# Optimization experiments

Hardware: AMD Instinct MI355X
Metric: run time of the kernel (lower is better)

Reference implementation:

```python
import jax, jax.numpy as jnp
import numpy as np

B, T, D = 4, 1024, 512
H, TD = 4, 5
DH = D // H          # per-head value dim
DFF = D // 2         # Clifford FFN half-width
DR = D               # reservoir size
M = 64               # 2**mem_depth leaves
OFFSETS = (-3, -2, -1, 0)  # causal sheaf window=3
EPS = 1e-5

def _ln(x, g, b):
    m = jnp.mean(x, axis=-1, keepdims=True)
    v = jnp.mean((x - m) ** 2, axis=-1, keepdims=True)
    return (x - m) / jnp.sqrt(v + EPS) * g + b

def setup_inputs() -> dict:
    keys = iter(jax.random.split(jax.random.key(0), 64))
    def rn(shape, s=0.02):
        return (jax.random.normal(next(keys), shape) * s).astype(jnp.float32)
    x = jax.random.normal(next(keys), (B, T, D), dtype=jnp.float32)
    # sparse reservoir recurrence matrix (sparsity=0.9)
    wres_mask = (jax.random.uniform(next(keys), (DR, DR)) > 0.9).astype(jnp.float32)
    res_Wres = jax.random.normal(next(keys), (DR, DR)) * wres_mask * 0.05
    eye = jnp.eye(D, dtype=jnp.float32)
    sheaf_Rw = jnp.stack([eye + rn((D, D), 0.01) for _ in OFFSETS])  # [4,D,D]
    return dict(
        x=x,
        ln1_g=jnp.ones((D,)), ln1_b=jnp.zeros((D,)),
        ln2_g=jnp.ones((D,)), ln2_b=jnp.zeros((D,)),
        ln3_g=jnp.ones((D,)), ln3_b=jnp.zeros((D,)),
        ln4_g=jnp.ones((D,)), ln4_b=jnp.zeros((D,)),
        attn_Wp=rn((H * TD, D)), attn_bp=jnp.zeros((H * TD,)),
        attn_Wv=rn((D, D)), attn_Wo=rn((D, D)),
        ffn_Wr=rn((DFF, D)), ffn_br=jnp.zeros((DFF,)),
        ffn_Wi=rn((DFF, D)), ffn_bi=jnp.zeros((DFF,)),
        ffn_Wg=rn((D, D)), ffn_bg=jnp.zeros((D,)),
        ffn_Wout=rn((D, D)), ffn_bout=jnp.zeros((D,)),
        res_Win=rn((DR, D)), res_Wres=res_Wres,
        res_logrho=jnp.float32(0.0), res_leak=jnp.float32(0.3),
        res_readout=rn((D, DR)),
        res_v0=jax.random.normal(next(keys), (DR,), dtype=jnp.float32),
        mem_keys=rn((M, D)), mem_vals=rn((M, D)),
        mem_Wq=rn((D, D)), mem_Wout=rn((D, D)), mem_bout=jnp.zeros((D,)),
        sheaf_Rw=sheaf_Rw, sheaf_Rb=jnp.zeros((len(OFFSETS), D)),
        sheaf_alpha=jnp.float32(0.15),
    )

def reference(x, ln1_g, ln1_b, ln2_g, ln2_b, ln3_g, ln3_b, ln4_g, ln4_b,
              attn_Wp, attn_bp, attn_Wv, attn_Wo,
              ffn_Wr, ffn_br, ffn_Wi, ffn_bi, ffn_Wg, ffn_bg, ffn_Wout, ffn_bout,
              res_Win, res_Wres, res_logrho, res_leak, res_readout, res_v0,
              mem_keys, mem_vals, mem_Wq, mem_Wout, mem_bout,
              sheaf_Rw, sheaf_Rb, sheaf_alpha):
    Bx, Tx, d = x.shape

    def attn_fn(h):  # PAdicAttention, causal
        paths = jax.nn.sigmoid(h @ attn_Wp.T + attn_bp)
        paths = paths.reshape(Bx, Tx, H, TD).transpose(0, 2, 1, 3)   # [B,H,T,TD]
        pq = paths[:, :, :, None, :]
        pk = paths[:, :, None, :, :]
        agree = pq * pk + (1.0 - pq) * (1.0 - pk)                    # [B,H,T,T,TD]
        sim = jnp.sum(jnp.cumprod(agree, axis=-1), axis=-1) / TD     # [B,H,T,T]
        mask = jnp.triu(jnp.ones((Tx, Tx), bool), 1)
        sim = jnp.where(mask[None, None], -jnp.inf, sim)
        a = jax.nn.softmax(sim, axis=-1)
        V = (h @ attn_Wv.T).reshape(Bx, Tx, H, DH).transpose(0, 2, 1, 3)
        ctx = jnp.einsum('bhqk,bhkd->bhqd', a, V)
        return ctx.transpose(0, 2, 1, 3).reshape(Bx, Tx, d) @ attn_Wo.T

    def res_fn(h):  # EchoStateReservoir
        rho_t = jax.nn.sigmoid(res_logrho) * 1.5
        Wd = jax.lax.stop_gradient(res_Wres)
        def pi(v, _):
            v = Wd @ v
            n = jnp.linalg.norm(v)
            return jnp.where(n > 0, v / n, v), None
        v, _ = jax.lax.scan(pi, res_v0, None, length=3)
        rho_c = jax.lax.stop_gradient(jnp.linalg.norm(Wd @ v))
        Ws = res_Wres * (rho_t / jnp.maximum(rho_c, 1e-6))
        lk = jax.nn.sigmoid(res_leak)
        u = h @ res_Win.T                                            # [B,T,dr]
        def step(hs, ut):
            hs = (1.0 - lk) * hs + lk * jnp.tanh(hs @ Ws.T + ut)
            return hs, hs
        _, Hs = jax.lax.scan(step, jnp.zeros((Bx, DR), x.dtype), u.transpose(1, 0, 2))
        return Hs.transpose(1, 0, 2) @ res_readout.T

    def mem_fn(h):  # PAdicMemory
        q = h @ mem_Wq.T
        w = jax.nn.softmax(q @ mem_keys.T / jnp.sqrt(jnp.float32(d)), axis=-1)
        return (w @ mem_vals) @ mem_Wout.T + mem_bout

    def ffn_fn(h):  # CliffordFFN
        r = h @ ffn_Wr.T + ffn_br
        i = h @ ffn_Wi.T + ffn_bi
        prod = jnp.concatenate([r * r - i * i, 2.0 * r * i], axis=-1)
        gate = jax.nn.sigmoid(h @ ffn_Wg.T + ffn_bg)
        return (prod * gate) @ ffn_Wout.T + ffn_bout

    def sheaf_fn(h):  # SheafDiffusion, causal offsets
        lap = jnp.zeros_like(h)
        for idx, delta in enumerate(OFFSETS):
            Rx = h @ sheaf_Rw[idx].T + sheaf_Rb[idx]
            if delta == 0:
                x_nb = h
            else:
                ad = -delta
                x_nb = jnp.concatenate(
                    [jnp.zeros((Bx, ad, d), h.dtype), h[:, :Tx - ad, :]], axis=1)
            lap = lap + (Rx - x_nb) @ sheaf_Rw[idx]   # note: @ W, not W.T (as in source)
        return h - jnp.abs(sheaf_alpha) * lap

    x = x + attn_fn(_ln(x, ln1_g, ln1_b))
    x = x + res_fn(_ln(x, ln2_g, ln2_b))
    x = x + mem_fn(_ln(x, ln3_g, ln3_b))
    x = x + ffn_fn(_ln(x, ln4_g, ln4_b))
    return sheaf_fn(x)
```

## Files before the change

### kernel.cpp

```cpp
#include <hip/hip_runtime.h>
#include <hip/hip_bf16.h>
#include <stdint.h>

typedef unsigned short u16;
typedef unsigned int u32;
typedef unsigned long long u64;
typedef __bf16 bf16x8 __attribute__((ext_vector_type(8)));
typedef float f32x4 __attribute__((ext_vector_type(4)));
typedef int i32x4 __attribute__((ext_vector_type(4)));

__device__ __forceinline__ u16 f2bf(float f){
  unsigned u = __float_as_uint(f);
  u += 0x7fffu + ((u>>16)&1u);
  return (u16)(u>>16);
}
__device__ __forceinline__ float sigm(float x){ return 1.f/(1.f+__expf(-x)); }
__device__ __forceinline__ float tanh_fast(float x){ float e = __expf(2.f*x); return 1.f - 2.f/(e+1.f); }

__device__ __forceinline__ void gl_lds16(const void* g, void* l){
  __builtin_amdgcn_global_load_lds((const __attribute__((address_space(1))) void*)g,
                                   (__attribute__((address_space(3))) void*)l, 16, 0, 0);
}

__global__ __launch_bounds__(128) void prep_weights(
  const float* Wp, const float* Wv, const float* Wo, const float* Win, const float* rd,
  const float* Wq, const float* keys, const float* vals, const float* mWo,
  const float* Wr, const float* Wi, const float* Wg, const float* fWo, const float* Rw,
  const float* bp, const float* fbr, const float* fbi, const float* fbg,
  u16* WpB, u16* WvB, u16* WoB, u16* WinB, u16* rdB,
  u16* WqB, u16* keysB, u16* valsB, u16* mWoB,
  u16* WrB, u16* WiB, u16* WgB, u16* fWoB, u16* RwB,
  float* bpp, float* bpc, float* ss)
{
  int blk = blockIdx.x, t = threadIdx.x;
  if(blk==6912){ if(t<128) bpp[t] = (t<20)? bp[t] : 0.f; return; }
  if(blk==6913){
    for(int j=t; j<1024; j+=128)
      bpc[j] = (j<256)? fbr[j] : (j<512)? fbi[j-256] : fbg[j-512];
    return;
  }
  if(blk==6914){ if(t==0) ss[0]=1.f; else if(t<5) ss[t]=0.f; return; }
  const float* src = nullptr; u16* dst = nullptr; int r;
  if(blk<128){ r=blk; dst=WpB+(size_t)r*512; if(r<20) src=Wp+(size_t)r*512; }
  else if(blk<640){ r=blk-128; dst=WvB+(size_t)r*512; src=Wv+(size_t)r*512; }
  else if(blk<1152){ r=blk-640; dst=WoB+(size_t)r*512; src=Wo+(size_t)r*512; }
  else if(blk<1664){ r=blk-1152; dst=WinB+(size_t)r*512; src=Win+(size_t)r*512; }
  else if(blk<2176){ r=blk-1664; dst=rdB+(size_t)r*512; src=rd+(size_t)r*512; }
  else if(blk<2688){ r=blk-2176; dst=WqB+(size_t)r*512; src=Wq+(size_t)r*512; }
  else if(blk<2752){ r=blk-2688; dst=keysB+(size_t)r*512; src=keys+(size_t)r*512; }
  else if(blk<2816){ r=blk-2752; dst=valsB+(size_t)r*512; src=vals+(size_t)r*512; }
  else if(blk<3328){ r=blk-2816; dst=mWoB+(size_t)r*512; src=mWo+(size_t)r*512; }
  else if(blk<3584){ r=blk-3328; dst=WrB+(size_t)r*512; src=Wr+(size_t)r*512; }
  else if(blk<3840){ r=blk-3584; dst=WiB+(size_t)r*512; src=Wi+(size_t)r*512; }
  else if(blk<4352){ r=blk-3840; dst=WgB+(size_t)r*512; src=Wg+(size_t)r*512; }
  else if(blk<4864){ r=blk-4352; dst=fWoB+(size_t)r*512; src=fWo+(size_t)r*512; }
  else { r=blk-4864; dst=RwB+(size_t)r*512; src=Rw+(size_t)r*512; }
  if(src){
    float4 a = *(const float4*)&src[t*4];
    ushort4 o; o.x=f2bf(a.x); o.y=f2bf(a.y); o.z=f2bf(a.z); o.w=f2bf(a.w);
    *(ushort4*)&dst[t*4] = o;
  } else {
    ushort4 z; z.x=0; z.y=0; z.z=0; z.w=0;
    *(ushort4*)&dst[t*4] = z;
  }
}

__global__ __launch_bounds__(256) void transpose_rw(const float* __restrict__ Rw, u16* __restrict__ RwT){
  __shared__ float tl[32][33];
  int z = blockIdx.z, it = blockIdx.x, jt = blockIdx.y;
  const float* src = Rw + (size_t)z*262144;
  u16* dst = RwT + (size_t)z*262144;
  int r = threadIdx.x>>3, c4 = (threadIdx.x&7)*4;
  float4 v = *(const float4*)&src[(size_t)(jt*32+r)*512 + it*32 + c4];
  tl[r][c4+0]=v.x; tl[r][c4+1]=v.y; tl[r][c4+2]=v.z; tl[r][c4+3]=v.w;
  __syncthreads();
  ushort4 o;
  o.x = f2bf(tl[c4+0][r]); o.y = f2bf(tl[c4+1][r]);
  o.z = f2bf(tl[c4+2][r]); o.w = f2bf(tl[c4+3][r]);
  *(ushort4*)&dst[(size_t)(it*32+r)*512 + jt*32 + c4] = o;
}

__global__ __launch_bounds__(64) void ln_kernel(const float* __restrict__ x, const float* __restrict__ g,
      const float* __restrict__ b, u16* __restrict__ out)
{
  int row = blockIdx.x, lane = threadIdx.x;
  const float* xr = x + (size_t)row*512;
  float4 v0 = *(const float4*)&xr[lane*4];
  float4 v1 = *(const float4*)&xr[256+lane*4];
  float s = v0.x+v0.y+v0.z+v0.w + v1.x+v1.y+v1.z+v1.w;
  float q = v0.x*v0.x+v0.y*v0.y+v0.z*v0.z+v0.w*v0.w + v1.x*v1.x+v1.y*v1.y+v1.z*v1.z+v1.w*v1.w;
  #pragma unroll
  for(int m=1;m<64;m<<=1){ s += __shfl_xor(s,m); q += __shfl_xor(q,m); }
  float mean = s*(1.f/512.f);
  float var  = q*(1.f/512.f) - mean*mean;
  float rstd = rsqrtf(var + 1e-5f);
  float4 g0 = *(const float4*)&g[lane*4], g1 = *(const float4*)&g[256+lane*4];
  float4 b0 = *(const float4*)&b[lane*4], b1 = *(const float4*)&b[256+lane*4];
  ushort4 o0, o1;
  o0.x = f2bf((v0.x-mean)*rstd*g0.x + b0.x); o0.y = f2bf((v0.y-mean)*rstd*g0.y + b0.y);
  o0.z = f2bf((v0.z-mean)*rstd*g0.z + b0.z); o0.w = f2bf((v0.w-mean)*rstd*g0.w + b0.w);
  o1.x = f2bf((v1.x-mean)*rstd*g1.x + b1.x); o1.y = f2bf((v1.y-mean)*rstd*g1.y + b1.y);
  o1.z = f2bf((v1.z-mean)*rstd*g1.z + b1.z); o1.w = f2bf((v1.w-mean)*rstd*g1.w + b1.w);
  *(ushort4*)&out[(size_t)row*512 + lane*4] = o0;
  *(ushort4*)&out[(size_t)row*512 + 256 + lane*4] = o1;
}

template<int EPI>
__global__ __launch_bounds__(256,2) void gemm_nt(
  const u16* __restrict__ A, const u16* __restrict__ Bw, int K, int ldc,
  float* __restrict__ outf, u16* __restrict__ outb,
  const float* __restrict__ bias, const float* __restrict__ resid,
  const float* __restrict__ aux, float* __restrict__ outf2,
  const float* __restrict__ scal, int shift_ad)
{
  __shared__ u16 Al[128*64];
  __shared__ u16 Bl[64*64];
  const int t = threadIdx.x;
  const int bm = blockIdx.x, bn = blockIdx.y;
  const int wid = t>>6, lane = t&63;
  const int wr = wid>>1, wc = wid&1;
  const int fr = lane&15, fq = lane>>4;
  f32x4 acc[4][2] = {};
  const int nK = K>>6;
  const u16* Ab = A + (size_t)(bm*128)*K;
  const u16* Bb = Bw + (size_t)(bn*64)*K;
  const int srow8 = t>>3;
  const int scol = (t&7)*8;
  char* AlB = (char*)Al; char* BlB = (char*)Bl;
  const int lbase = wid*1024;
  for(int bk=0; bk<nK; ++bk){
    #pragma unroll
    for(int c=0;c<4;++c)
      gl_lds16(&Ab[(size_t)(c*32+srow8)*K + bk*64 + scol], AlB + c*4096 + lbase);
    #pragma unroll
    for(int c=0;c<2;++c)
      gl_lds16(&Bb[(size_t)(c*32+srow8)*K + bk*64 + scol], BlB + c*4096 + lbase);
    __syncthreads();
    #pragma unroll
    for(int kk=0;kk<2;++kk){
      bf16x8 af[4], bf[2];
      #pragma unroll
      for(int m=0;m<4;++m) af[m] = *(const bf16x8*)&Al[(wr*64+m*16+fr)*64 + kk*32 + fq*8];
      #pragma unroll
      for(int n=0;n<2;++n) bf[n] = *(const bf16x8*)&Bl[(wc*32+n*16+fr)*64 + kk*32 + fq*8];
      #pragma unroll
      for(int m=0;m<4;++m)
        #pragma unroll
        for(int n=0;n<2;++n)
          acc[m][n] = __builtin_amdgcn_mfma_f32_16x16x32_bf16(af[m], bf[n], acc[m][n], 0,0,0);
    }
    __syncthreads();
  }
  float alpha = 0.f;
  if(EPI==8) alpha = fabsf(scal[0]);
  #pragma unroll
  for(int m=0;m<4;++m){
    int gr0 = bm*128 + wr*64 + m*16 + fq*4;
    #pragma unroll
    for(int n=0;n<2;++n){
      int gc = bn*64 + wc*32 + n*16 + fr;
      float bv = 0.f;
      if(EPI==2||EPI==3||EPI==5||EPI==6||EPI==7||EPI==9) bv = bias[gc];
      if(EPI==10 && gc<128) bv = bias[gc];
      #pragma unroll
      for(int i=0;i<4;++i){
        int r = gr0 + i;
        float v = acc[m][n][i] + bv;
        if(EPI==3) v = sigm(v);
        if(EPI==1||EPI==5||EPI==6) v += resid[(size_t)r*ldc + gc];
        if(EPI==7){
          int ts = r & 1023;
          float xnb = (ts >= shift_ad) ? aux[(size_t)(r-shift_ad)*ldc + gc] : 0.f;
          v -= xnb;
        }
        if(EPI==8){
          outf[(size_t)r*ldc + gc] -= alpha*v;
        } else if(EPI==9){
          if(gc<512) outf[(size_t)r*512 + gc] = v;
          else       outf2[(size_t)r*512 + gc-512] = sigm(v);
        } else if(EPI==10){
          if(gc<128) outf[(size_t)r*128 + gc] = sigm(v);
          else       outf2[(size_t)r*512 + gc-128] = v;
        } else {
          if(EPI==0||EPI==1||EPI==2||EPI==3||EPI==5||EPI==6) outf[(size_t)r*ldc + gc] = v;
          if(EPI==6) outf2[(size_t)r*ldc + gc] = v;
          if(EPI==4||EPI==6||EPI==7) outb[(size_t)r*ldc + gc] = f2bf(v);
        }
      }
    }
  }
}

__global__ __launch_bounds__(128) void attn_kernel(
  const float* __restrict__ paths, const float* __restrict__ Vbuf, u16* __restrict__ ctxb)
{
  const int t = threadIdx.x;
  const int qt = blockIdx.x, bh = blockIdx.y;
  const int b = bh>>2, h = bh&3;
  const int rb = b<<10;
  const int ql = t>>2, sub = t&3;
  const int q = qt*32 + ql;
  const int wid = t>>6, lane = t&63;
  const int fr = lane&15, fq = lane>>4;
  __shared__ u16 Vl[128][72];
  __shared__ u16 Pl[32][72];
  __shared__ float pkl[64][6];
  __shared__ float scl[32];
  __shared__ float lsm[32];
  float al[5], bl[5];
  #pragma unroll
  for(int l=0;l<5;++l){
    float p = paths[(size_t)(rb+q)*128 + h*5 + l];
    al[l] = 2.f*p - 1.f; bl[l] = 1.f - p;
  }
  float m_run = -1e30f, l_run = 0.f;
  f32x4 acc[2][4] = {};
  const int nkt = (qt>>1) + 1;
  for(int kt=0; kt<nkt; ++kt){
    int k0 = kt*64;
    for(int i=t; i<320; i+=128){
      int k = i/5, l = i%5;
      pkl[k][l] = paths[(size_t)(rb+k0+k)*128 + h*5 + l];
    }
    {
      int dg = (t&31)*4, kbase = t>>5;
      #pragma unroll
      for(int i=0;i<16;++i){
        int k = kbase + i*4;
        float4 v4 = *(const float4*)&Vbuf[(size_t)(rb+k0+k)*512 + h*128 + dg];
        Vl[dg+0][k] = f2bf(v4.x); Vl[dg+1][k] = f2bf(v4.y);
        Vl[dg+2][k] = f2bf(v4.z); Vl[dg+3][k] = f2bf(v4.w);
      }
    }
    __syncthreads();
    float pj[16]; float tm = -1e30f;
    #pragma unroll
    for(int j=0;j<16;++j){
      int kidx = sub*16 + j;
      int k = k0 + kidx;
      float s;
      if(k <= q){
        float c = al[0]*pkl[kidx][0] + bl[0];
        float sa = c;
        #pragma unroll
        for(int l=1;l<5;++l){ c *= al[l]*pkl[kidx][l] + bl[l]; sa += c; }
        s = sa*0.2f;
      } else s = -1e30f;
      pj[j] = s; tm = fmaxf(tm, s);
    }
    tm = fmaxf(tm, __shfl_xor(tm,1,4));
    tm = fmaxf(tm, __shfl_xor(tm,2,4));
    float m_new = fmaxf(m_run, tm);
    float corr = __expf(m_run - m_new);
    float ls = 0.f;
    #pragma unroll
    for(int j=0;j<16;++j){
      float p = (pj[j] > -1e29f) ? __expf(pj[j]-m_new) : 0.f;
      ls += p;
      Pl[ql][sub*16+j] = f2bf(p);
    }
    l_run = l_run*corr + ls;
    m_run = m_new;
    if(sub==0) scl[ql] = corr;
    __syncthreads();
    #pragma unroll
    for(int m=0;m<2;++m){
      float c0 = scl[m*16+fq*4+0], c1 = scl[m*16+fq*4+1];
      float c2 = scl[m*16+fq*4+2], c3 = scl[m*16+fq*4+3];
      #pragma unroll
      for(int n=0;n<4;++n){ acc[m][n][0]*=c0; acc[m][n][1]*=c1; acc[m][n][2]*=c2; acc[m][n][3]*=c3; }
    }
    #pragma unroll
    for(int kk=0;kk<2;++kk){
      bf16x8 af[2], bf[4];
      #pragma unroll
      for(int m=0;m<2;++m) af[m] = *(const bf16x8*)&Pl[m*16+fr][kk*32+fq*8];
      #pragma unroll
      for(int n=0;n<4;++n) bf[n] = *(const bf16x8*)&Vl[wid*64+n*16+fr][kk*32+fq*8];
      #pragma unroll
      for(int m=0;m<2;++m)
        #pragma unroll
        for(int n=0;n<4;++n)
          acc[m][n] = __builtin_amdgcn_mfma_f32_16x16x32_bf16(af[m], bf[n], acc[m][n], 0,0,0);
    }
    __syncthreads();
  }
  {
    float lt = l_run + __shfl_xor(l_run,1,4);
    lt += __shfl_xor(lt,2,4);
    if(sub==0) lsm[ql] = lt;
  }
  __syncthreads();
  #pragma unroll
  for(int m=0;m<2;++m){
    float inv[4];
    #pragma unroll
    for(int i=0;i<4;++i) inv[i] = 1.f/lsm[m*16+fq*4+i];
    #pragma unroll
    for(int n=0;n<4;++n){
      int row = rb + qt*32 + m*16 + fq*4;
      int col = h*128 + wid*64 + n*16 + fr;
      #pragma unroll
      for(int i=0;i<4;++i)
        ctxb[(size_t)(row+i)*512 + col] = f2bf(acc[m][n][i]*inv[i]);
    }
  }
}

__global__ __launch_bounds__(256) void pmv(const float* __restrict__ W, const float* __restrict__ vin,
                    const float* __restrict__ ssin, float* __restrict__ vout, float* __restrict__ ssout)
{
  __shared__ float vs[512];
  int t = threadIdx.x;
  int j = blockIdx.x*16 + (t>>4), ks = t&15;
  float s = ssin[0];
  float inv = (s>0.f)? rsqrtf(s) : 1.f;
  vs[t] = vin[t]*inv; vs[t+256] = vin[t+256]*inv;
  __syncthreads();
  float p = 0.f;
  const float* wr = &W[(size_t)j*512 + ks*32];
  #pragma unroll
  for(int kk=0;kk<32;++kk) p += wr[kk]*vs[ks*32+kk];
  p += __shfl_xor(p,1,16); p += __shfl_xor(p,2,16); p += __shfl_xor(p,4,16); p += __shfl_xor(p,8,16);
  if(ks==0){ vout[j] = p; atomicAdd(ssout, p*p); }
}

__global__ __launch_bounds__(128) void scale_ws(const float* __restrict__ Wres, const float* __restrict__ ss4,
                         const float* __restrict__ logrho, signed char* __restrict__ WsQ,
                         float* __restrict__ wscale)
{
  __shared__ float wmax[2];
  int j = blockIdx.x, t = threadIdx.x;
  float rho_t = 1.5f * sigm(logrho[0]);
  float rho_c = sqrtf(ss4[0]);
  float sc = rho_t / fmaxf(rho_c, 1e-6f);
  float4 w = *(const float4*)&Wres[(size_t)j*512 + t*4];
  w.x*=sc; w.y*=sc; w.z*=sc; w.w*=sc;
  float m = fmaxf(fmaxf(fabsf(w.x),fabsf(w.y)), fmaxf(fabsf(w.z),fabsf(w.w)));
  #pragma unroll
  for(int d=1; d<64; d<<=1) m = fmaxf(m, __shfl_xor(m, d));
  if((t&63)==0) wmax[t>>6] = m;
  __syncthreads();
  float rm = fmaxf(wmax[0], wmax[1]);
  float qs = (rm > 0.f) ? rm*(1.f/127.f) : 1.f;
  float inv = 1.f/qs;
  int q0 = __float2int_rn(w.x*inv), q1 = __float2int_rn(w.y*inv);
  int q2 = __float2int_rn(w.z*inv), q3 = __float2int_rn(w.w*inv);
  q0 = min(127,max(-127,q0)); q1 = min(127,max(-127,q1));
  q2 = min(127,max(-127,q2)); q3 = min(127,max(-127,q3));
  u32 pk = (u32)(q0&0xff) | ((u32)(q1&0xff)<<8) | ((u32)(q2&0xff)<<16) | ((u32)(q3&0xff)<<24);
  *(u32*)&WsQ[(size_t)j*512 + t*4] = pk;
  if(t==0) wscale[j] = qs*(1.f/127.f);
}

__global__ __launch_bounds__(512) void scan_kernel(
  const signed char* __restrict__ WsQ, const float* __restrict__ wscale,
  const float* __restrict__ u, const float* __restrict__ leak_p,
  u16* __restrict__ HsB)
{
  const int t = threadIdx.x;
  const int w = t>>6, lane = t&63, fr = lane&15, fq = lane>>4;
  const int colb = w*64;
  const float lk = sigm(leak_p[0]);
  const float omlk = 1.f - lk;
  __shared__ signed char Sl[2][16*512];
  for(int i=t; i<4096; i+=512) ((u32*)Sl)[i] = 0u;
  float mysc[4];
  i32x4 bw[4][8];
  #pragma unroll
  for(int cg=0; cg<4; ++cg){
    int col = colb + cg*16 + fr;
    mysc[cg] = wscale[col];
    #pragma unroll
    for(int ks=0; ks<8; ++ks)
      bw[cg][ks] = *(const i32x4*)&WsQ[(size_t)col*512 + ks*64 + fq*16];
  }
  #pragma unroll
  for(int cg=0; cg<4; ++cg)
    #pragma unroll
    for(int ks=0; ks<8; ++ks)
      asm volatile("" : "+v"(bw[cg][ks]));
  float hp[4];
  #pragma unroll
  for(int cg=0;cg<4;++cg) hp[cg]=0.f;
  float uvc[4];
  #pragma unroll
  for(int cg=0;cg<4;++cg)
    uvc[cg] = u[(size_t)(fq*1024)*512 + colb + cg*16 + fr];
  const int rdswz = ((fr&3)<<4) ^ (((fr>>2)&3)<<6);
  const int wrswz = fq<<6;
  __syncthreads();
  for(int ts=0; ts<1024; ++ts){
    const int tn = (ts+1 < 1024) ? (ts+1) : 1023;
    float uvn[4];
    #pragma unroll
    for(int cg=0;cg<4;++cg)
      uvn[cg] = u[(size_t)(fq*1024 + tn)*512 + colb + cg*16 + fr];
    const signed char* Sb = Sl[ts&1];
    i32x4 af[8];
    #pragma unroll
    for(int ks=0; ks<8; ++ks)
      af[ks] = *(const i32x4*)&Sb[fr*512 + ((ks*64 + fq*16) ^ rdswz)];
    i32x4 accA[4], accB[4];
    #pragma unroll
    for(int cg=0;cg<4;++cg){ i32x4 z = {0,0,0,0}; accA[cg] = z; accB[cg] = z; }
    #pragma unroll
    for(int ks=0;ks<4;++ks)
      #pragma unroll
      for(int cg=0;cg<4;++cg){
        accA[cg] = __builtin_amdgcn_mfma_i32_16x16x64_i8(af[ks],   bw[cg][ks],   accA[cg], 0,0,0);
        accB[cg] = __builtin_amdgcn_mfma_i32_16x16x64_i8(af[ks+4], bw[cg][ks+4], accB[cg], 0,0,0);
      }
    signed char* So = Sl[(ts+1)&1];
    #pragma unroll
    for(int cg=0;cg<4;++cg){
      float pre = (float)(accA[cg][0] + accB[cg][0])*mysc[cg] + uvc[cg];
      float h = omlk*hp[cg] + lk*tanh_fast(pre);
      hp[cg] = h;
      int qi = __float2int_rn(h*127.f);
      qi = min(127, max(-127, qi));
      So[(4*fq)*512 + ((colb + cg*16 + fr) ^ wrswz)] = (signed char)qi;
      HsB[(size_t)(fq*1024+ts)*512 + colb + cg*16 + fr] = f2bf(h);
      uvc[cg] = uvn[cg];
    }
    asm volatile("s_waitcnt lgkmcnt(0)" ::: "memory");
    __builtin_amdgcn_s_barrier();
    asm volatile("" ::: "memory");
  }
}

__global__ __launch_bounds__(256) void mem_kernel(
  const u16* __restrict__ qb, const u16* __restrict__ keysB, const u16* __restrict__ valsB,
  u16* __restrict__ ctx2b)
{
  const int t = threadIdx.x, rt = blockIdx.x;
  const int wid = t>>6, lane = t&63, fr = lane&15, fq = lane>>4;
  __shared__ float S[64][65];
  __shared__ u16 Pl[64][72];
  __shared__ u16 VT[256][72];
  {
    f32x4 accs[4] = {};
    for(int ks=0; ks<16; ++ks){
      bf16x8 bfrag = *(const bf16x8*)&keysB[(size_t)(wid*16+fr)*512 + ks*32 + fq*8];
      #pragma unroll
      for(int mt=0;mt<4;++mt){
        bf16x8 afrag = *(const bf16x8*)&qb[(size_t)(rt*64+mt*16+fr)*512 + ks*32 + fq*8];
        accs[mt] = __builtin_amdgcn_mfma_f32_16x16x32_bf16(afrag, bfrag, accs[mt], 0,0,0);
      }
    }
    #pragma unroll
    for(int mt=0;mt<4;++mt)
      #pragma unroll
      for(int i=0;i<4;++i)
        S[mt*16+fq*4+i][wid*16+fr] = accs[mt][i];
  }
  __syncthreads();
  if(t<64){
    float m = -1e30f;
    for(int j=0;j<64;++j) m = fmaxf(m, S[t][j]);
    const float scale = 0.04419417382f;
    float sum = 0.f;
    for(int j=0;j<64;++j){ float p = __expf((S[t][j]-m)*scale); sum += p; S[t][j] = p; }
    float inv = 1.f/sum;
    for(int j=0;j<64;++j) Pl[t][j] = f2bf(S[t][j]*inv);
  }
  __syncthreads();
  for(int pass=0; pass<2; ++pass){
    {
      int k = t&63, cb = t>>6;
      #pragma unroll
      for(int i=0;i<8;++i){
        int d0 = (cb + i*4)*8;
        uint4 v = *(const uint4*)&valsB[(size_t)k*512 + pass*256 + d0];
        VT[d0+0][k]=(u16)(v.x); VT[d0+1][k]=(u16)(v.x>>16);
        VT[d0+2][k]=(u16)(v.y); VT[d0+3][k]=(u16)(v.y>>16);
        VT[d0+4][k]=(u16)(v.z); VT[d0+5][k]=(u16)(v.z>>16);
        VT[d0+6][k]=(u16)(v.w); VT[d0+7][k]=(u16)(v.w>>16);
      }
    }
    __syncthreads();
    f32x4 accp[4][4] = {};
    #pragma unroll
    for(int kk=0;kk<2;++kk){
      bf16x8 af[4], bf[4];
      #pragma unroll
      for(int mt=0;mt<4;++mt) af[mt] = *(const bf16x8*)&Pl[mt*16+fr][kk*32+fq*8];
      #pragma unroll
      for(int nt=0;nt<4;++nt) bf[nt] = *(const bf16x8*)&VT[wid*64+nt*16+fr][kk*32+fq*8];
      #pragma unroll
      for(int mt=0;mt<4;++mt)
        #pragma unroll
        for(int nt=0;nt<4;++nt)
          accp[mt][nt] = __builtin_amdgcn_mfma_f32_16x16x32_bf16(af[mt], bf[nt], accp[mt][nt], 0,0,0);
    }
    #pragma unroll
    for(int mt=0;mt<4;++mt)
      #pragma unroll
      for(int nt=0;nt<4;++nt){
        int row = rt*64 + mt*16 + fq*4;
        int col = pass*256 + wid*64 + nt*16 + fr;
        #pragma unroll
        for(int i=0;i<4;++i)
          ctx2b[(size_t)(row+i)*512 + col] = f2bf(accp[mt][nt][i]);
      }
    __syncthreads();
  }
}

__global__ __launch_bounds__(256) void prodgate(const float* __restrict__ ri, const float* __restrict__ g,
                         u16* __restrict__ pgb)
{
  int gi = blockIdx.x*256 + threadIdx.x;
  int row = gi>>7, c4 = (gi&127)*4;
  const float* base = ri + (size_t)row*512;
  float4 gv = *(const float4*)&g[(size_t)row*512 + c4];
  float4 o;
  if(c4 < 256){
    float4 r = *(const float4*)&base[c4];
    float4 ii = *(const float4*)&base[256+c4];
    o.x = (r.x*r.x - ii.x*ii.x)*gv.x; o.y = (r.y*r.y - ii.y*ii.y)*gv.y;
    o.z = (r.z*r.z - ii.z*ii.z)*gv.z; o.w = (r.w*r.w - ii.w*ii.w)*gv.w;
  } else {
    float4 r = *(const float4*)&base[c4-256];
    float4 ii = *(const float4*)&base[c4];
    o.x = 2.f*r.x*ii.x*gv.x; o.y = 2.f*r.y*ii.y*gv.y;
    o.z = 2.f*r.z*ii.z*gv.z; o.w = 2.f*r.w*ii.w*gv.w;
  }
  ushort4 us; us.x=f2bf(o.x); us.y=f2bf(o.y); us.z=f2bf(o.z); us.w=f2bf(o.w);
  *(ushort4*)&pgb[(size_t)row*512 + c4] = us;
}

static void launch_gemm(int epi, dim3 grid, const u16* A, const u16* B, int ldc,
  float* outf, u16* outb, const float* bias, const float* resid, const float* aux,
  float* outf2, const float* scal, int ad, hipStream_t s)
{
  switch(epi){
    case 0: gemm_nt<0><<<grid,256,0,s>>>(A,B,512,ldc,outf,outb,bias,resid,aux,outf2,scal,ad); break;
    case 1: gemm_nt<1><<<grid,256,0,s>>>(A,B,512,ldc,outf,outb,bias,resid,aux,outf2,scal,ad); break;
    case 2: gemm_nt<2><<<grid,256,0,s>>>(A,B,512,ldc,outf,outb,bias,resid,aux,outf2,scal,ad); break;
    case 3: gemm_nt<3><<<grid,256,0,s>>>(A,B,512,ldc,outf,outb,bias,resid,aux,outf2,scal,ad); break;
    case 4: gemm_nt<4><<<grid,256,0,s>>>(A,B,512,ldc,outf,outb,bias,resid,aux,outf2,scal,ad); break;
    case 5: gemm_nt<5><<<grid,256,0,s>>>(A,B,512,ldc,outf,outb,bias,resid,aux,outf2,scal,ad); break;
    case 6: gemm_nt<6><<<grid,256,0,s>>>(A,B,512,ldc,outf,outb,bias,resid,aux,outf2,scal,ad); break;
    case 7: gemm_nt<7><<<grid,256,0,s>>>(A,B,512,ldc,outf,outb,bias,resid,aux,outf2,scal,ad); break;
    case 8: gemm_nt<8><<<grid,256,0,s>>>(A,B,512,ldc,outf,outb,bias,resid,aux,outf2,scal,ad); break;
    case 9: gemm_nt<9><<<grid,256,0,s>>>(A,B,512,ldc,outf,outb,bias,resid,aux,outf2,scal,ad); break;
    case 10: gemm_nt<10><<<grid,256,0,s>>>(A,B,512,ldc,outf,outb,bias,resid,aux,outf2,scal,ad); break;
  }
}

extern "C" void kernel_launch(void* const* d_in, const int* in_sizes, int n_in,
                              void* d_out, int out_size, void* d_ws, size_t ws_size,
                              hipStream_t stream)
{
  const float* x      = (const float*)d_in[0];
  const float* ln1g   = (const float*)d_in[1];  const float* ln1b = (const float*)d_in[2];
  const float* ln2g   = (const float*)d_in[3];  const float* ln2b = (const float*)d_in[4];
  const float* ln3g   = (const float*)d_in[5];  const float* ln3b = (const float*)d_in[6];
  const float* ln4g   = (const float*)d_in[7];  const float* ln4b = (const float*)d_in[8];
  const float* aWp    = (const float*)d_in[9];  const float* abp  = (const float*)d_in[10];
  const float* aWv    = (const float*)d_in[11]; const float* aWo  = (const float*)d_in[12];
  const float* fWr    = (const float*)d_in[13]; const float* fbr  = (const float*)d_in[14];
  const float* fWi    = (const float*)d_in[15]; const float* fbi  = (const float*)d_in[16];
  const float* fWg    = (const float*)d_in[17]; const float* fbg  = (const float*)d_in[18];
  const float* fWo    = (const float*)d_in[19]; const float* fbo  = (const float*)d_in[20];
  const float* rWin   = (const float*)d_in[21]; const float* rWres= (const float*)d_in[22];
  const float* rlogr  = (const float*)d_in[23]; const float* rleak= (const float*)d_in[24];
  const float* rread  = (const float*)d_in[25]; const float* rv0  = (const float*)d_in[26];
  const float* mkeys  = (const float*)d_in[27]; const float* mvals= (const float*)d_in[28];
  const float* mWq    = (const float*)d_in[29]; const float* mWo  = (const float*)d_in[30];
  const float* mbo    = (const float*)d_in[31];
  const float* sRw    = (const float*)d_in[32]; const float* sRb  = (const float*)d_in[33];
  const float* salpha = (const float*)d_in[34];
  (void)in_sizes; (void)n_in; (void)out_size;

  char* ws = (char*)d_ws;
  float* XCUR  = (float*)(ws + 0);
  u16*   HB    = (u16*)  (ws + 8388608);
  float* VU    = (float*)(ws + 12582912);
  u16*   X4B   = (u16*)  (ws + 12582912);
  float* PATHS = (float*)(ws + 20971520);
  u16*   CTXB  = (u16*)  (ws + 23068672);
  u16*   HSB   = (u16*)  (ws + 27262976);
  char* WB = ws + 31457280;
  u16* WpB   = (u16*)(WB + 0);
  u16* WvB   = (u16*)(WB + 131072);
  u16* WoB   = (u16*)(WB + 655360);
  u16* WinB  = (u16*)(WB + 1179648);
  u16* rdB   = (u16*)(WB + 1703936);
  u16* WqB   = (u16*)(WB + 2228224);
  u16* keysB = (u16*)(WB + 2752512);
  u16* valsB = (u16*)(WB + 2818048);
  u16* mWoB  = (u16*)(WB + 2883584);
  u16* WrB   = (u16*)(WB + 3407872);
  u16* WiB   = (u16*)(WB + 3670016);
  u16* WgB   = (u16*)(WB + 3932160);
  u16* fWoB  = (u16*)(WB + 4456448);
  u16* RwB   = (u16*)(WB + 4980736);
  u16* RwTB  = (u16*)(WB + 7077888);
  signed char* WsQ = (signed char*)(WB + 9175040);
  float* wscale = (float*)(WB + 9437184);
  float* bpp = (float*)(WB + 9699328);
  float* bpc = (float*)(WB + 9699840);
  float* ssv = (float*)(WB + 9733632);
  float* vr  = (float*)(WB + 9733696);
  float* GATE = (float*)d_out;

  if(ws_size < (size_t)41200000) return;

  prep_weights<<<6915,128,0,stream>>>(aWp,aWv,aWo,rWin,rread,mWq,mkeys,mvals,mWo,fWr,fWi,fWg,fWo,sRw,
      abp, fbr, fbi, fbg,
      WpB,WvB,WoB,WinB,rdB,WqB,keysB,valsB,mWoB,WrB,WiB,WgB,fWoB,RwB,bpp,bpc,ssv);
  transpose_rw<<<dim3(16,16,4),256,0,stream>>>(sRw, RwTB);

  dim3 g512(32,8), g640(32,10), g1024(32,16);

  ln_kernel<<<4096,64,0,stream>>>(x, ln1g, ln1b, HB);
  launch_gemm(10, g640, HB, WpB, 0, PATHS, nullptr, bpp, nullptr, nullptr, VU, nullptr, 0, stream);
  attn_kernel<<<dim3(32,16),128,0,stream>>>(PATHS, VU, CTXB);
  launch_gemm(1, g512, CTXB, WoB, 512, XCUR, nullptr, nullptr, x, nullptr, nullptr, nullptr, 0, stream);

  ln_kernel<<<4096,64,0,stream>>>(XCUR, ln2g, ln2b, HB);
  launch_gemm(0, g512, HB, WinB, 512, VU, nullptr, nullptr, nullptr, nullptr, nullptr, nullptr, 0, stream);
  pmv<<<32,256,0,stream>>>(rWres, rv0,   &ssv[0], &vr[0],    &ssv[1]);
  pmv<<<32,256,0,stream>>>(rWres, &vr[0],   &ssv[1], &vr[512],  &ssv[2]);
  pmv<<<32,256,0,stream>>>(rWres, &vr[512], &ssv[2], &vr[1024], &ssv[3]);
  pmv<<<32,256,0,stream>>>(rWres, &vr[1024],&ssv[3], &vr[1536], &ssv[4]);
  scale_ws<<<512,128,0,stream>>>(rWres, &ssv[4], rlogr, WsQ, wscale);
  scan_kernel<<<1,512,0,stream>>>(WsQ, wscale, VU, rleak, HSB);
  launch_gemm(1, g512, HSB, rdB, 512, XCUR, nullptr, nullptr, XCUR, nullptr, nullptr, nullptr, 0, stream);

  ln_kernel<<<4096,64,0,stream>>>(XCUR, ln3g, ln3b, HB);
  launch_gemm(4, g512, HB, WqB, 512, nullptr, CTXB, nullptr, nullptr, nullptr, nullptr, nullptr, 0, stream);
  mem_kernel<<<64,256,0,stream>>>(CTXB, keysB, valsB, HSB);
  launch_gemm(5, g512, HSB, mWoB, 512, XCUR, nullptr, mbo, XCUR, nullptr, nullptr, nullptr, 0, stream);

  ln_kernel<<<4096,64,0,stream>>>(XCUR, ln4g, ln4b, HB);
  launch_gemm(9, g1024, HB, WrB, 0, VU, nullptr, bpc, nullptr, nullptr, GATE, nullptr, 0, stream);
  prodgate<<<2048,256,0,stream>>>(VU, GATE, CTXB);
  launch_gemm(6, g512, CTXB, fWoB, 512, XCUR, X4B, fbo, XCUR, nullptr, (float*)d_out, nullptr, 0, stream);

  const int ads[4] = {3,2,1,0};
  for(int idx=0; idx<4; ++idx){
    launch_gemm(7, g512, X4B, RwB + (size_t)idx*262144, 512,
                nullptr, CTXB, sRb + idx*512, nullptr, XCUR, nullptr, nullptr, ads[idx], stream);
    launch_gemm(8, g512, CTXB, RwTB + (size_t)idx*262144, 512,
                (float*)d_out, nullptr, nullptr, nullptr, nullptr, nullptr, salpha, 0, stream);
  }
}
```

Baseline: 1.352 ms.

## Batch sheaf diffusion into two wide GEMMs and vectorize reservoir scan I/O

The four per-offset pairs of sheaf GEMMs become one N=2048 GEMM that writes the shifted differences in bf16, followed by one K=2048 GEMM against a concatenated transposed Rw. This cuts the launch count and removes repeated read-modify-write passes over the fp32 output. The reservoir input projection and readout weights are column-permuted so the scan kernel can use float4 loads, packed int8 LDS stores and packed bf16 stores. The trade-off is that the neighbour term now comes from bf16 X4B instead of fp32 XCUR, which adds precision loss, and the change touches buffer aliasing.

```diff
diff --git a/kernel.cpp b/kernel.cpp
--- a/kernel.cpp
+++ b/kernel.cpp
@@ -14,6 +14,7 @@
   u += 0x7fffu + ((u>>16)&1u);
   return (u16)(u>>16);
 }
+__device__ __forceinline__ float bf2f(u16 h){ return __uint_as_float((u32)h<<16); }
 __device__ __forceinline__ float sigm(float x){ return 1.f/(1.f+__expf(-x)); }
 __device__ __forceinline__ float tanh_fast(float x){ float e = __expf(2.f*x); return 1.f - 2.f/(e+1.f); }
 
@@ -21,6 +22,7 @@
   __builtin_amdgcn_global_load_lds((const __attribute__((address_space(1))) void*)g,
                                    (__attribute__((address_space(3))) void*)l, 16, 0, 0);
 }
+
 
 __global__ __launch_bounds__(128) void prep_weights(
   const float* Wp, const float* Wv, const float* Wo, const float* Win, const float* rd,
@@ -41,11 +43,12 @@
   }
   if(blk==6914){ if(t==0) ss[0]=1.f; else if(t<5) ss[t]=0.f; return; }
   const float* src = nullptr; u16* dst = nullptr; int r;
+  bool perm = false;
   if(blk<128){ r=blk; dst=WpB+(size_t)r*512; if(r<20) src=Wp+(size_t)r*512; }
   else if(blk<640){ r=blk-128; dst=WvB+(size_t)r*512; src=Wv+(size_t)r*512; }
   else if(blk<1152){ r=blk-640; dst=WoB+(size_t)r*512; src=Wo+(size_t)r*512; }
   else if(blk<1664){ r=blk-1152; dst=WinB+(size_t)r*512; src=Win+(size_t)r*512; }
-  else if(blk<2176){ r=blk-1664; dst=rdB+(size_t)r*512; src=rd+(size_t)r*512; }
+  else if(blk<2176){ r=blk-1664; dst=rdB+(size_t)r*512; src=rd+(size_t)r*512; perm=true; }
   else if(blk<2688){ r=blk-2176; dst=WqB+(size_t)r*512; src=Wq+(size_t)r*512; }
   else if(blk<2752){ r=blk-2688; dst=keysB+(size_t)r*512; src=keys+(size_t)r*512; }
   else if(blk<2816){ r=blk-2752; dst=valsB+(size_t)r*512; src=vals+(size_t)r*512; }
@@ -58,7 +61,13 @@
   if(src){
     float4 a = *(const float4*)&src[t*4];
     ushort4 o; o.x=f2bf(a.x); o.y=f2bf(a.y); o.z=f2bf(a.z); o.w=f2bf(a.w);
-    *(ushort4*)&dst[t*4] = o;
+    if(perm){
+      int k0 = t*4;
+      int base = (k0 & ~63) | ((k0&15)<<2) | ((k0>>4)&3);
+      dst[base] = o.x; dst[base+4] = o.y; dst[base+8] = o.z; dst[base+12] = o.w;
+    } else {
+      *(ushort4*)&dst[t*4] = o;
+    }
   } else {
     ushort4 z; z.x=0; z.y=0; z.z=0; z.w=0;
     *(ushort4*)&dst[t*4] = z;
@@ -69,7 +78,6 @@
   __shared__ float tl[32][33];
   int z = blockIdx.z, it = blockIdx.x, jt = blockIdx.y;
   const float* src = Rw + (size_t)z*262144;
-  u16* dst = RwT + (size_t)z*262144;
   int r = threadIdx.x>>3, c4 = (threadIdx.x&7)*4;
   float4 v = *(const float4*)&src[(size_t)(jt*32+r)*512 + it*32 + c4];
   tl[r][c4+0]=v.x; tl[r][c4+1]=v.y; tl[r][c4+2]=v.z; tl[r][c4+3]=v.w;
@@ -77,7 +85,7 @@
   ushort4 o;
   o.x = f2bf(tl[c4+0][r]); o.y = f2bf(tl[c4+1][r]);
   o.z = f2bf(tl[c4+2][r]); o.w = f2bf(tl[c4+3][r]);
-  *(ushort4*)&dst[(size_t)(it*32+r)*512 + jt*32 + c4] = o;
+  *(ushort4*)&RwT[(size_t)(it*32+r)*2048 + z*512 + jt*32 + c4] = o;
 }
 
 __global__ __launch_bounds__(64) void ln_kernel(const float* __restrict__ x, const float* __restrict__ g,
@@ -160,7 +168,7 @@
     for(int n=0;n<2;++n){
       int gc = bn*64 + wc*32 + n*16 + fr;
       float bv = 0.f;
-      if(EPI==2||EPI==3||EPI==5||EPI==6||EPI==7||EPI==9) bv = bias[gc];
+      if(EPI==2||EPI==3||EPI==5||EPI==6||EPI==9||EPI==12) bv = bias[gc];
       if(EPI==10 && gc<128) bv = bias[gc];
       #pragma unroll
       for(int i=0;i<4;++i){
@@ -168,11 +176,6 @@
         float v = acc[m][n][i] + bv;
         if(EPI==3) v = sigm(v);
         if(EPI==1||EPI==5||EPI==6) v += resid[(size_t)r*ldc + gc];
-        if(EPI==7){
-          int ts = r & 1023;
-          float xnb = (ts >= shift_ad) ? aux[(size_t)(r-shift_ad)*ldc + gc] : 0.f;
-          v -= xnb;
-        }
         if(EPI==8){
           outf[(size_t)r*ldc + gc] -= alpha*v;
         } else if(EPI==9){
@@ -181,10 +184,20 @@
         } else if(EPI==10){
           if(gc<128) outf[(size_t)r*128 + gc] = sigm(v);
           else       outf2[(size_t)r*512 + gc-128] = v;
+        } else if(EPI==11){
+          int pc = (gc & ~63) | ((gc&15)<<2) | ((gc>>4)&3);
+          outf[(size_t)r*512 + pc] = v;
+        } else if(EPI==12){
+          int idx = gc>>9;
+          int ad = 3 - idx;
+          int ts = r & 1023;
+          float xnb = 0.f;
+          if(ts >= ad) xnb = bf2f(((const u16*)aux)[(size_t)(r-ad)*512 + (gc&511)]);
+          outb[(size_t)r*2048 + gc] = f2bf(v - xnb);
         } else {
-          if(EPI==0||EPI==1||EPI==2||EPI==3||EPI==5||EPI==6) outf[(size_t)r*ldc + gc] = v;
+          if(EPI==0||EPI==1||EPI==2||EPI==3||EPI==5) outf[(size_t)r*ldc + gc] = v;
           if(EPI==6) outf2[(size_t)r*ldc + gc] = v;
-          if(EPI==4||EPI==6||EPI==7) outb[(size_t)r*ldc + gc] = f2bf(v);
+          if(EPI==4||EPI==6) outb[(size_t)r*ldc + gc] = f2bf(v);
         }
       }
     }
@@ -331,12 +344,14 @@
 {
   __shared__ float wmax[2];
   int j = blockIdx.x, t = threadIdx.x;
+  int fr = t&15, blk = t>>4;
   float rho_t = 1.5f * sigm(logrho[0]);
   float rho_c = sqrtf(ss4[0]);
   float sc = rho_t / fmaxf(rho_c, 1e-6f);
-  float4 w = *(const float4*)&Wres[(size_t)j*512 + t*4];
-  w.x*=sc; w.y*=sc; w.z*=sc; w.w*=sc;
-  float m = fmaxf(fmaxf(fabsf(w.x),fabsf(w.y)), fmaxf(fabsf(w.z),fabsf(w.w)));
+  float w[4];
+  #pragma unroll
+  for(int cg=0;cg<4;++cg) w[cg] = Wres[(size_t)j*512 + blk*64 + cg*16 + fr]*sc;
+  float m = fmaxf(fmaxf(fabsf(w[0]),fabsf(w[1])), fmaxf(fabsf(w[2]),fabsf(w[3])));
   #pragma unroll
   for(int d=1; d<64; d<<=1) m = fmaxf(m, __shfl_xor(m, d));
   if((t&63)==0) wmax[t>>6] = m;
@@ -344,12 +359,12 @@
   float rm = fmaxf(wmax[0], wmax[1]);
   float qs = (rm > 0.f) ? rm*(1.f/127.f) : 1.f;
   float inv = 1.f/qs;
-  int q0 = __float2int_rn(w.x*inv), q1 = __float2int_rn(w.y*inv);
-  int q2 = __float2int_rn(w.z*inv), q3 = __float2int_rn(w.w*inv);
+  int q0 = __float2int_rn(w[0]*inv), q1 = __float2int_rn(w[1]*inv);
+  int q2 = __float2int_rn(w[2]*inv), q3 = __float2int_rn(w[3]*inv);
   q0 = min(127,max(-127,q0)); q1 = min(127,max(-127,q1));
   q2 = min(127,max(-127,q2)); q3 = min(127,max(-127,q3));
   u32 pk = (u32)(q0&0xff) | ((u32)(q1&0xff)<<8) | ((u32)(q2&0xff)<<16) | ((u32)(q3&0xff)<<24);
-  *(u32*)&WsQ[(size_t)j*512 + t*4] = pk;
+  *(u32*)&WsQ[(size_t)j*512 + blk*64 + fr*4] = pk;
   if(t==0) wscale[j] = qs*(1.f/127.f);
 }
 
@@ -383,19 +398,14 @@
   float hp[4];
   #pragma unroll
   for(int cg=0;cg<4;++cg) hp[cg]=0.f;
-  float uvc[4];
-  #pragma unroll
-  for(int cg=0;cg<4;++cg)
-    uvc[cg] = u[(size_t)(fq*1024)*512 + colb + cg*16 + fr];
+  const float* up = u + (size_t)(fq*1024)*512 + colb + fr*4;
+  u16* hsp = HsB + (size_t)(fq*1024)*512 + colb + fr*4;
+  float4 uvc = *(const float4*)up;  up += 512;
   const int rdswz = ((fr&3)<<4) ^ (((fr>>2)&3)<<6);
-  const int wrswz = fq<<6;
+  const int woff = (4*fq)*512 + ((colb + fr*4) ^ (fq<<6));
   __syncthreads();
   for(int ts=0; ts<1024; ++ts){
-    const int tn = (ts+1 < 1024) ? (ts+1) : 1023;
-    float uvn[4];
-    #pragma unroll
-    for(int cg=0;cg<4;++cg)
-      uvn[cg] = u[(size_t)(fq*1024 + tn)*512 + colb + cg*16 + fr];
+    float4 uvn = *(const float4*)up;  up += 512;
     const signed char* Sb = Sl[ts&1];
     i32x4 af[8];
     #pragma unroll
@@ -411,18 +421,24 @@
         accA[cg] = __builtin_amdgcn_mfma_i32_16x16x64_i8(af[ks],   bw[cg][ks],   accA[cg], 0,0,0);
         accB[cg] = __builtin_amdgcn_mfma_i32_16x16x64_i8(af[ks+4], bw[cg][ks+4], accB[cg], 0,0,0);
       }
-    signed char* So = Sl[(ts+1)&1];
+    float h[4];
+    float uu[4] = {uvc.x, uvc.y, uvc.z, uvc.w};
     #pragma unroll
     for(int cg=0;cg<4;++cg){
-      float pre = (float)(accA[cg][0] + accB[cg][0])*mysc[cg] + uvc[cg];
-      float h = omlk*hp[cg] + lk*tanh_fast(pre);
-      hp[cg] = h;
-      int qi = __float2int_rn(h*127.f);
-      qi = min(127, max(-127, qi));
-      So[(4*fq)*512 + ((colb + cg*16 + fr) ^ wrswz)] = (signed char)qi;
-      HsB[(size_t)(fq*1024+ts)*512 + colb + cg*16 + fr] = f2bf(h);
-      uvc[cg] = uvn[cg];
-    }
+      float pre = (float)(accA[cg][0] + accB[cg][0])*mysc[cg] + uu[cg];
+      h[cg] = omlk*hp[cg] + lk*tanh_fast(pre);
+      hp[cg] = h[cg];
+    }
+    int q0 = __float2int_rn(h[0]*127.f), q1 = __float2int_rn(h[1]*127.f);
+    int q2 = __float2int_rn(h[2]*127.f), q3 = __float2int_rn(h[3]*127.f);
+    u32 qp = (u32)(q0&0xff) | ((u32)(q1&0xff)<<8) | ((u32)(q2&0xff)<<16) | ((u32)q3<<24);
+    *(u32*)&Sl[(ts+1)&1][woff] = qp;
+    u32 p01, p23;
+    asm volatile("v_cvt_pk_bf16_f32 %0, %1, %2" : "=v"(p01) : "v"(h[0]), "v"(h[1]));
+    asm volatile("v_cvt_pk_bf16_f32 %0, %1, %2" : "=v"(p23) : "v"(h[2]), "v"(h[3]));
+    uint2 hv; hv.x = p01; hv.y = p23;
+    *(uint2*)hsp = hv;  hsp += 512;
+    uvc = uvn;
     asm volatile("s_waitcnt lgkmcnt(0)" ::: "memory");
     __builtin_amdgcn_s_barrier();
     asm volatile("" ::: "memory");
@@ -530,22 +546,21 @@
   *(ushort4*)&pgb[(size_t)row*512 + c4] = us;
 }
 
-static void launch_gemm(int epi, dim3 grid, const u16* A, const u16* B, int ldc,
+static void launch_gemm(int epi, dim3 grid, const u16* A, const u16* B, int K, int ldc,
   float* outf, u16* outb, const float* bias, const float* resid, const float* aux,
   float* outf2, const float* scal, int ad, hipStream_t s)
 {
   switch(epi){
-    case 0: gemm_nt<0><<<grid,256,0,s>>>(A,B,512,ldc,outf,outb,bias,resid,aux,outf2,scal,ad); break;
-    case 1: gemm_nt<1><<<grid,256,0,s>>>(A,B,512,ldc,outf,outb,bias,resid,aux,outf2,scal,ad); break;
-    case 2: gemm_nt<2><<<grid,256,0,s>>>(A,B,512,ldc,outf,outb,bias,resid,aux,outf2,scal,ad); break;
-    case 3: gemm_nt<3><<<grid,256,0,s>>>(A,B,512,ldc,outf,outb,bias,resid,aux,outf2,scal,ad); break;
-    case 4: gemm_nt<4><<<grid,256,0,s>>>(A,B,512,ldc,outf,outb,bias,resid,aux,outf2,scal,ad); break;
-    case 5: gemm_nt<5><<<grid,256,0,s>>>(A,B,512,ldc,outf,outb,bias,resid,aux,outf2,scal,ad); break;
-    case 6: gemm_nt<6><<<grid,256,0,s>>>(A,B,512,ldc,outf,outb,bias,resid,aux,outf2,scal,ad); break;
-    case 7: gemm_nt<7><<<grid,256,0,s>>>(A,B,512,ldc,outf,outb,bias,resid,aux,outf2,scal,ad); break;
-    case 8: gemm_nt<8><<<grid,256,0,s>>>(A,B,512,ldc,outf,outb,bias,resid,aux,outf2,scal,ad); break;
-    case 9: gemm_nt<9><<<grid,256,0,s>>>(A,B,512,ldc,outf,outb,bias,resid,aux,outf2,scal,ad); break;
-    case 10: gemm_nt<10><<<grid,256,0,s>>>(A,B,512,ldc,outf,outb,bias,resid,aux,outf2,scal,ad); break;
+    case 0: gemm_nt<0><<<grid,256,0,s>>>(A,B,K,ldc,outf,outb,bias,resid,aux,outf2,scal,ad); break;
+    case 1: gemm_nt<1><<<grid,256,0,s>>>(A,B,K,ldc,outf,outb,bias,resid,aux,outf2,scal,ad); break;
+    case 4: gemm_nt<4><<<grid,256,0,s>>>(A,B,K,ldc,outf,outb,bias,resid,aux,outf2,scal,ad); break;
+    case 5: gemm_nt<5><<<grid,256,0,s>>>(A,B,K,ldc,outf,outb,bias,resid,aux,outf2,scal,ad); break;
+    case 6: gemm_nt<6><<<grid,256,0,s>>>(A,B,K,ldc,outf,outb,bias,resid,aux,outf2,scal,ad); break;
+    case 8: gemm_nt<8><<<grid,256,0,s>>>(A,B,K,ldc,outf,outb,bias,resid,aux,outf2,scal,ad); break;
+    case 9: gemm_nt<9><<<grid,256,0,s>>>(A,B,K,ldc,outf,outb,bias,resid,aux,outf2,scal,ad); break;
+    case 10: gemm_nt<10><<<grid,256,0,s>>>(A,B,K,ldc,outf,outb,bias,resid,aux,outf2,scal,ad); break;
+    case 11: gemm_nt<11><<<grid,256,0,s>>>(A,B,K,ldc,outf,outb,bias,resid,aux,outf2,scal,ad); break;
+    case 12: gemm_nt<12><<<grid,256,0,s>>>(A,B,K,ldc,outf,outb,bias,resid,aux,outf2,scal,ad); break;
   }
 }
 
@@ -576,9 +591,10 @@
 
   char* ws = (char*)d_ws;
   float* XCUR  = (float*)(ws + 0);
+  u16*   X4B   = (u16*)  (ws + 8388608);
   u16*   HB    = (u16*)  (ws + 8388608);
   float* VU    = (float*)(ws + 12582912);
-  u16*   X4B   = (u16*)  (ws + 12582912);
+  u16*   TBUF  = (u16*)  (ws + 12582912);
   float* PATHS = (float*)(ws + 20971520);
   u16*   CTXB  = (u16*)  (ws + 23068672);
   u16*   HSB   = (u16*)  (ws + 27262976);
@@ -613,38 +629,33 @@
       WpB,WvB,WoB,WinB,rdB,WqB,keysB,valsB,mWoB,WrB,WiB,WgB,fWoB,RwB,bpp,bpc,ssv);
   transpose_rw<<<dim3(16,16,4),256,0,stream>>>(sRw, RwTB);
 
-  dim3 g512(32,8), g640(32,10), g1024(32,16);
+  dim3 g512(32,8), g640(32,10), g1024(32,16), g2048(32,32);
 
   ln_kernel<<<4096,64,0,stream>>>(x, ln1g, ln1b, HB);
-  launch_gemm(10, g640, HB, WpB, 0, PATHS, nullptr, bpp, nullptr, nullptr, VU, nullptr, 0, stream);
+  launch_gemm(10, g640, HB, WpB, 512, 0, PATHS, nullptr, bpp, nullptr, nullptr, VU, nullptr, 0, stream);
   attn_kernel<<<dim3(32,16),128,0,stream>>>(PATHS, VU, CTXB);
-  launch_gemm(1, g512, CTXB, WoB, 512, XCUR, nullptr, nullptr, x, nullptr, nullptr, nullptr, 0, stream);
+  launch_gemm(1, g512, CTXB, WoB, 512, 512, XCUR, nullptr, nullptr, x, nullptr, nullptr, nullptr, 0, stream);
 
   ln_kernel<<<4096,64,0,stream>>>(XCUR, ln2g, ln2b, HB);
-  launch_gemm(0, g512, HB, WinB, 512, VU, nullptr, nullptr, nullptr, nullptr, nullptr, nullptr, 0, stream);
+  launch_gemm(11, g512, HB, WinB, 512, 512, VU, nullptr, nullptr, nullptr, nullptr, nullptr, nullptr, 0, stream);
   pmv<<<32,256,0,stream>>>(rWres, rv0,   &ssv[0], &vr[0],    &ssv[1]);
   pmv<<<32,256,0,stream>>>(rWres, &vr[0],   &ssv[1], &vr[512],  &ssv[2]);
   pmv<<<32,256,0,stream>>>(rWres, &vr[512], &ssv[2], &vr[1024], &ssv[3]);
   pmv<<<32,256,0,stream>>>(rWres, &vr[1024],&ssv[3], &vr[1536], &ssv[4]);
   scale_ws<<<512,128,0,stream>>>(rWres, &ssv[4], rlogr, WsQ, wscale);
   scan_kernel<<<1,512,0,stream>>>(WsQ, wscale, VU, rleak, HSB);
-  launch_gemm(1, g512, HSB, rdB, 512, XCUR, nullptr, nullptr, XCUR, nullptr, nullptr, nullptr, 0, stream);
+  launch_gemm(1, g512, HSB, rdB, 512, 512, XCUR, nullptr, nullptr, XCUR, nullptr, nullptr, nullptr, 0, stream);
 
   ln_kernel<<<4096,64,0,stream>>>(XCUR, ln3g, ln3b, HB);
-  launch_gemm(4, g512, HB, WqB, 512, nullptr, CTXB, nullptr, nullptr, nullptr, nullptr, nullptr, 0, stream);
+  launch_gemm(4, g512, HB, WqB, 512, 512, nullptr, CTXB, nullptr, nullptr, nullptr, nullptr, nullptr, 0, stream);
   mem_kernel<<<64,256,0,stream>>>(CTXB, keysB, valsB, HSB);
-  launch_gemm(5, g512, HSB, mWoB, 512, XCUR, nullptr, mbo, XCUR, nullptr, nullptr, nullptr, 0, stream);
+  launch_gemm(5, g512, HSB, mWoB, 512, 512, XCUR, nullptr, mbo, XCUR, nullptr, nullptr, nullptr, 0, stream);
 
   ln_kernel<<<4096,64,0,stream>>>(XCUR, ln4g, ln4b, HB);
-  launch_gemm(9, g1024, HB, WrB, 0, VU, nullptr, bpc, nullptr, nullptr, GATE, nullptr, 0, stream);
+  launch_gemm(9, g1024, HB, WrB, 512, 0, VU, nullptr, bpc, nullptr, nullptr, GATE, nullptr, 0, stream);
   prodgate<<<2048,256,0,stream>>>(VU, GATE, CTXB);
-  launch_gemm(6, g512, CTXB, fWoB, 512, XCUR, X4B, fbo, XCUR, nullptr, (float*)d_out, nullptr, 0, stream);
-
-  const int ads[4] = {3,2,1,0};
-  for(int idx=0; idx<4; ++idx){
-    launch_gemm(7, g512, X4B, RwB + (size_t)idx*262144, 512,
-                nullptr, CTXB, sRb + idx*512, nullptr, XCUR, nullptr, nullptr, ads[idx], stream);
-    launch_gemm(8, g512, CTXB, RwTB + (size_t)idx*262144, 512,
-                (float*)d_out, nullptr, nullptr, nullptr, nullptr, nullptr, salpha, 0, stream);
-  }
-}
+  launch_gemm(6, g512, CTXB, fWoB, 512, 512, nullptr, X4B, fbo, XCUR, nullptr, (float*)d_out, nullptr, 0, stream);
+
+  launch_gemm(12, g2048, X4B, RwB, 512, 0, nullptr, TBUF, sRb, nullptr, (const float*)X4B, nullptr, nullptr, 0, stream);
+  launch_gemm(8, g512, TBUF, RwTB, 2048, 512, (float*)d_out, nullptr, nullptr, nullptr, nullptr, nullptr, salpha, 0, stream);
+}
```

New measurement: 1.203 ms. 11.0% less time.
